# Kernel tuning notes

Hardware: AMD Instinct MI355X
Metric: run time of the kernel (lower is better)

The kernel has to match this reference:

```python
import jax, jax.numpy as jnp
import numpy as np

B, C, H, W = 4, 512, 64, 64
CI = C // 2  # inter_channel


def setup_inputs() -> dict:
    key = jax.random.key(0)
    ks = jax.random.split(key, 5)
    x = jax.random.normal(ks[0], (B, C, H, W), dtype=jnp.float32)
    # 1x1 convs with bias=False == channel-mixing matrices (out_ch, in_ch)
    w_phi = jax.random.normal(ks[1], (CI, C), dtype=jnp.float32) * 0.02
    w_theta = jax.random.normal(ks[2], (CI, C), dtype=jnp.float32) * 0.02
    w_g = jax.random.normal(ks[3], (CI, C), dtype=jnp.float32) * 0.02
    w_mask = jax.random.normal(ks[4], (C, CI), dtype=jnp.float32) * 0.02
    return {"x": x, "w_phi": w_phi, "w_theta": w_theta, "w_g": w_g, "w_mask": w_mask}


def reference(x, w_phi, w_theta, w_g, w_mask):
    b, c, h, w = x.shape
    n = h * w
    ci = w_phi.shape[0]
    xf = x.reshape(b, c, n)  # (b, c, N)
    # 1x1 convs as channel matmuls -> (b, ci, N)
    phi = jnp.einsum('oc,bcn->bon', w_phi, xf)
    theta = jnp.einsum('oc,bcn->bon', w_theta, xf)
    g = jnp.einsum('oc,bcn->bon', w_g, xf)
    # f = theta^T @ phi : (b, N, N), unscaled scores
    f = jnp.einsum('bcn,bcm->bnm', theta, phi)
    a = jax.nn.softmax(f, axis=-1)
    # y = a @ g^T, produced directly in (b, ci, N) layout (fuses the permute)
    y = jnp.einsum('bnm,bcm->bcn', a, g)
    # conv_mask: 1x1 conv back to C channels
    out = jnp.einsum('oc,bcn->bon', w_mask, y)
    return out.reshape(b, c, h, w)
```

## Files before the change

kernel.cpp:

```cpp
#include <hip/hip_runtime.h>


#define BB 4
#define CC 512
#define NN_SP 4096
#define CI 256

typedef _Float16 f16x8 __attribute__((ext_vector_type(8)));
typedef float f32x4 __attribute__((ext_vector_type(4)));

__device__ __forceinline__ void async16(const void* gsrc, void* ldst) {
  __builtin_amdgcn_global_load_lds(
      (const __attribute__((address_space(1))) unsigned int*)gsrc,
      (__attribute__((address_space(3))) unsigned int*)ldst, 16, 0, 0);
}

__global__ __launch_bounds__(256) void convert_w(
    const float* __restrict__ wphi, const float* __restrict__ wtheta,
    const float* __restrict__ wg, const float* __restrict__ wmask,
    _Float16* __restrict__ wpt, _Float16* __restrict__ wgh, _Float16* __restrict__ wmh) {
  int i = blockIdx.x * 256 + threadIdx.x;
  if (i < 512 * 512) {
    int row = i >> 9, k = i & 511;
    float v = (row < 256) ? wphi[row * 512 + k] : wtheta[(row - 256) * 512 + k];
    wpt[i] = (_Float16)v;
  } else if (i < 512 * 512 + 256 * 512) {
    int j = i - 512 * 512;
    wgh[j] = (_Float16)wg[j];
  } else {
    int j = i - 512 * 512 - 256 * 512;
    wmh[j] = (_Float16)wmask[j];
  }
}

__global__ __launch_bounds__(256) void transpose_x(const float* __restrict__ x,
                                                   _Float16* __restrict__ xT) {
  __shared__ float tile[64][65];
  const int n0 = blockIdx.x * 64, c0 = blockIdx.y * 64, b = blockIdx.z;
  const int tx = threadIdx.x & 63, ty = threadIdx.x >> 6;
  const float* xb = x + (long long)b * CC * NN_SP;
#pragma unroll
  for (int i = 0; i < 16; ++i) {
    int row = i * 4 + ty;
    tile[row][tx] = xb[(long long)(c0 + row) * NN_SP + n0 + tx];
  }
  __syncthreads();
  const int cx = threadIdx.x & 31;
  const int ny = threadIdx.x >> 5;
  _Float16* xTb = xT + (long long)b * NN_SP * CC;
#pragma unroll
  for (int i = 0; i < 8; ++i) {
    int n = i * 8 + ny;
    union { _Float16 h[2]; unsigned int u; } pk;
    pk.h[0] = (_Float16)tile[cx * 2][n];
    pk.h[1] = (_Float16)tile[cx * 2 + 1][n];
    *(unsigned int*)(xTb + (long long)(n0 + n) * CC + c0 + cx * 2) = pk.u;
  }
}

template <int M, int NT, int K, bool F16OUT>
__global__ __launch_bounds__(256, 2) void gemm_bt(
    const _Float16* __restrict__ Ab, const _Float16* __restrict__ Btb,
    void* __restrict__ Cb, long long sA, long long sB, long long sC) {
  __shared__ _Float16 As[128 * 64];
  __shared__ _Float16 Bs[128 * 64];
  const int tid = threadIdx.x, lane = tid & 63, w = tid >> 6;
  const int wm = w >> 1, wn = w & 1;
  const int l15 = lane & 15, lq = lane >> 4;
  const int b = blockIdx.z;
  const _Float16* A = Ab + (long long)b * sA;
  const _Float16* Bt = Btb + (long long)b * sB;
  const int m0 = blockIdx.y * 128, n0 = blockIdx.x * 128;

  f32x4 acc[4][4];
#pragma unroll
  for (int i = 0; i < 4; ++i)
#pragma unroll
    for (int j = 0; j < 4; ++j) acc[i][j] = (f32x4){0.f, 0.f, 0.f, 0.f};

  for (int k0 = 0; k0 < K; k0 += 64) {
    __syncthreads();
#pragma unroll
    for (int j = 0; j < 4; ++j) {
      int chw = j * 256 + w * 64;
      int ch = chw + lane;
      int us = ch ^ ((ch >> 3) & 7);
      int row = us >> 3, kc = us & 7;
      async16(A + (long long)(m0 + row) * K + k0 + kc * 8, (void*)(As + chw * 8));
      async16(Bt + (long long)(n0 + row) * K + k0 + kc * 8, (void*)(Bs + chw * 8));
    }
    __syncthreads();
#pragma unroll
    for (int kh = 0; kh < 2; ++kh) {
      f16x8 af[4], bf[4];
#pragma unroll
      for (int mt = 0; mt < 4; ++mt) {
        int c = (wm * 64 + mt * 16 + l15) * 8 + kh * 4 + lq;
        af[mt] = *(const f16x8*)(As + (c ^ ((c >> 3) & 7)) * 8);
      }
#pragma unroll
      for (int nt = 0; nt < 4; ++nt) {
        int c = (wn * 64 + nt * 16 + l15) * 8 + kh * 4 + lq;
        bf[nt] = *(const f16x8*)(Bs + (c ^ ((c >> 3) & 7)) * 8);
      }
#pragma unroll
      for (int mt = 0; mt < 4; ++mt)
#pragma unroll
        for (int nt = 0; nt < 4; ++nt)
          acc[mt][nt] = __builtin_amdgcn_mfma_f32_16x16x32_f16(af[mt], bf[nt], acc[mt][nt], 0, 0, 0);
    }
  }

#pragma unroll
  for (int mt = 0; mt < 4; ++mt)
#pragma unroll
    for (int nt = 0; nt < 4; ++nt)
#pragma unroll
      for (int r = 0; r < 4; ++r) {
        int row = m0 + wm * 64 + mt * 16 + lq * 4 + r;
        int col = n0 + wn * 64 + nt * 16 + l15;
        if (F16OUT)
          ((_Float16*)Cb + (long long)b * sC)[(long long)row * NT + col] = (_Float16)acc[mt][nt][r];
        else
          ((float*)Cb + (long long)b * sC)[(long long)row * NT + col] = acc[mt][nt][r];
      }
}

__global__ __launch_bounds__(512, 2) void flash_attn3(
    const _Float16* __restrict__ pt, const _Float16* __restrict__ g,
    _Float16* __restrict__ yT) {
  __shared__ _Float16 Stg[2][2][16384];
  __shared__ _Float16 Ps[8][2048];
  const int tid = threadIdx.x, lane = tid & 63, w = tid >> 6;
  const int hw = w >> 2, wp = w & 3;
  const int l15 = lane & 15, lq = lane >> 4;

  const int idx = blockIdx.x;
  const int b = (idx >> 1) & 3;
  const int q0 = (((idx >> 3) << 1) | (idx & 1)) * 64;
  const int kvbase = hw * 2048;
  const _Float16* __restrict__ ptb = pt + (long long)b * NN_SP * 512;
  const _Float16* __restrict__ gb = g + (long long)b * CI * NN_SP;

  int offPhi[4], offG[4], chw_[4];
#pragma unroll
  for (int j = 0; j < 4; ++j) {
    int u = wp * 256 + j * 64 + lane;
    chw_[j] = wp * 256 + j * 64;
    int us = u ^ ((u >> 3) & 7);
    int k2 = us >> 9, nv8 = (us >> 6) & 7, r15 = (us >> 2) & 15, rq = us & 3;
    offPhi[j] = (nv8 * 16 + r15) * 512 + k2 * 32 + rq * 8;
    int kq = us >> 8, ct4 = (us >> 6) & 3;
    offG[j] = (ct4 * 16 + r15) * 4096 + kq * 32 + rq * 8;
  }
  const int rswz = (l15 * 4 + lq) ^ ((l15 >> 1) & 7);

  f16x8 qreg[8];
#pragma unroll
  for (int kk = 0; kk < 8; ++kk)
    qreg[kk] = *(const f16x8*)(
        ptb + (long long)(q0 + wp * 16 + l15) * 512 + 256 + kk * 32 + lq * 8);

  f16x8 onesf;
#pragma unroll
  for (int j = 0; j < 8; ++j) onesf[j] = (_Float16)1.f;

  f32x4 yacc[16];
#pragma unroll
  for (int nt = 0; nt < 16; ++nt) yacc[nt] = (f32x4){0.f, 0.f, 0.f, 0.f};
  f32x4 lacc = (f32x4){0.f, 0.f, 0.f, 0.f};
  float mrow[4] = {-3e38f, -3e38f, -3e38f, -3e38f};

  auto issue = [&](int mq, int bi) {
    if (mq >= 64) return;
    int t = mq >> 2, mp = mq & 3, kv0 = kvbase + t * 128;
#pragma unroll
    for (int hh = 0; hh < 2; ++hh) {
      int sub = mp * 2 + hh;
      _Float16* buf = Stg[hw][bi] + hh * 8192;
      if (sub < 4) {
        const _Float16* basep = ptb + (long long)kv0 * 512 + sub * 64;
#pragma unroll
        for (int j = 0; j < 4; ++j)
          async16(basep + offPhi[j], (void*)(buf + chw_[j] * 8));
      } else {
        const _Float16* baseg = gb + (long long)(sub - 4) * 64 * 4096 + kv0;
#pragma unroll
        for (int j = 0; j < 4; ++j)
          async16(baseg + offG[j], (void*)(buf + chw_[j] * 8));
      }
    }
  };

  int p = 0;
  issue(0, 0);

  for (int t = 0; t < 16; ++t) {
    f32x4 S[8];
#pragma unroll
    for (int i = 0; i < 8; ++i) S[i] = (f32x4){0.f, 0.f, 0.f, 0.f};

#pragma unroll
    for (int mp = 0; mp < 2; ++mp) {
      asm volatile("s_waitcnt vmcnt(0)" ::: "memory");
      asm volatile("s_barrier" ::: "memory");
      issue(p + 1, (p + 1) & 1);
      const _Float16* bufb = Stg[hw][p & 1];
      __builtin_amdgcn_s_setprio(1);
#pragma unroll
      for (int hh = 0; hh < 2; ++hh) {
        int c = mp * 2 + hh;
        const _Float16* buf = bufb + hh * 8192;
#pragma unroll
        for (int k2 = 0; k2 < 2; ++k2)
#pragma unroll
          for (int nv = 0; nv < 8; ++nv) {
            f16x8 bf = *(const f16x8*)(buf + (k2 * 512 + nv * 64 + rswz) * 8);
            S[nv] = __builtin_amdgcn_mfma_f32_16x16x32_f16(qreg[c * 2 + k2], bf, S[nv], 0, 0, 0);
          }
      }
      __builtin_amdgcn_s_setprio(0);
      ++p;
    }

    float nm[4];
    int grew = 0;
#pragma unroll
    for (int r = 0; r < 4; ++r) {
      float mx = fmaxf(fmaxf(S[0][r], S[1][r]), fmaxf(S[2][r], S[3][r]));
      mx = fmaxf(mx, fmaxf(fmaxf(S[4][r], S[5][r]), fmaxf(S[6][r], S[7][r])));
#pragma unroll
      for (int d = 1; d < 16; d <<= 1) mx = fmaxf(mx, __shfl_xor(mx, d, 64));
      nm[r] = fmaxf(mrow[r], mx);
      grew |= (mx > mrow[r]);
    }
    if (__ballot(grew)) {
      f32x4 al;
#pragma unroll
      for (int r = 0; r < 4; ++r) {
        al[r] = __expf(mrow[r] - nm[r]);
        mrow[r] = nm[r];
      }
#pragma unroll
      for (int nt = 0; nt < 16; ++nt) yacc[nt] *= al;
      lacc *= al;
    }
#pragma unroll
    for (int r = 0; r < 4; ++r)
#pragma unroll
      for (int nv = 0; nv < 8; ++nv) S[nv][r] = __expf(S[nv][r] - mrow[r]);

#pragma unroll
    for (int nv = 0; nv < 8; ++nv) {
      int kq = nv >> 1;
      int lqr = (nv & 1) * 2 + (l15 >> 3);
      int e = l15 & 7;
#pragma unroll
      for (int r = 0; r < 4; ++r) {
        int u = kq * 64 + lqr * 16 + lq * 4 + r;
        int us = u ^ ((u >> 3) & 7);
        Ps[w][us * 8 + e] = (_Float16)S[nv][r];
      }
    }
    f16x8 aP[4];
#pragma unroll
    for (int kq = 0; kq < 4; ++kq) {
      int ur = kq * 64 + lane;
      int urs = ur ^ ((ur >> 3) & 7);
      aP[kq] = *(const f16x8*)(&Ps[w][urs * 8]);
    }

#pragma unroll
    for (int kq = 0; kq < 4; ++kq)
      lacc = __builtin_amdgcn_mfma_f32_16x16x32_f16(aP[kq], onesf, lacc, 0, 0, 0);

#pragma unroll
    for (int mp = 0; mp < 2; ++mp) {
      asm volatile("s_waitcnt vmcnt(0)" ::: "memory");
      asm volatile("s_barrier" ::: "memory");
      issue(p + 1, (p + 1) & 1);
      const _Float16* bufb = Stg[hw][p & 1];
      __builtin_amdgcn_s_setprio(1);
#pragma unroll
      for (int hh = 0; hh < 2; ++hh) {
        int cg = mp * 2 + hh;
        const _Float16* buf = bufb + hh * 8192;
#pragma unroll
        for (int kq = 0; kq < 4; ++kq)
#pragma unroll
          for (int ct = 0; ct < 4; ++ct) {
            f16x8 bf = *(const f16x8*)(buf + (kq * 256 + ct * 64 + rswz) * 8);
            yacc[cg * 4 + ct] =
                __builtin_amdgcn_mfma_f32_16x16x32_f16(aP[kq], bf, yacc[cg * 4 + ct], 0, 0, 0);
          }
      }
      __builtin_amdgcn_s_setprio(0);
      ++p;
    }
  }

  __syncthreads();
  float* mbuf = (float*)Stg;
  float* sbuf = (float*)((char*)Stg + 81920);
  if (hw == 1) {
#pragma unroll
    for (int r = 0; r < 4; ++r) {
      int rr = wp * 16 + lq * 4 + r;
#pragma unroll
      for (int nt = 0; nt < 16; ++nt)
        mbuf[rr * 257 + nt * 16 + l15] = yacc[nt][r];
      if (l15 == 0) {
        sbuf[rr * 2 + 0] = mrow[r];
        sbuf[rr * 2 + 1] = lacc[r];
      }
    }
  }
  __syncthreads();
  if (hw == 0) {
    _Float16* yTb = yT + (long long)b * NN_SP * CI;
#pragma unroll
    for (int r = 0; r < 4; ++r) {
      int rr = wp * 16 + lq * 4 + r;
      float m2 = sbuf[rr * 2 + 0], l2 = sbuf[rr * 2 + 1];
      float m = fmaxf(mrow[r], m2);
      float w1 = __expf(mrow[r] - m), w2 = __expf(m2 - m);
      float inv = 1.f / (w1 * lacc[r] + w2 * l2);
      int row = q0 + rr;
#pragma unroll
      for (int nt = 0; nt < 16; ++nt) {
        float v2 = mbuf[rr * 257 + nt * 16 + l15];
        yTb[(long long)row * CI + nt * 16 + l15] =
            (_Float16)((w1 * yacc[nt][r] + w2 * v2) * inv);
      }
    }
  }
}

extern "C" void kernel_launch(void* const* d_in, const int* in_sizes, int n_in,
                              void* d_out, int out_size, void* d_ws, size_t ws_size,
                              hipStream_t stream) {
  const float* x = (const float*)d_in[0];
  const float* w_phi = (const float*)d_in[1];
  const float* w_theta = (const float*)d_in[2];
  const float* w_g = (const float*)d_in[3];
  const float* w_mask = (const float*)d_in[4];
  float* out = (float*)d_out;
  char* ws = (char*)d_ws;

  _Float16* xT = (_Float16*)(ws);
  _Float16* pt = (_Float16*)(ws + 16777216);
  _Float16* gB = (_Float16*)(ws + 33554432);
  _Float16* yT = (_Float16*)(ws + 41943040);
  _Float16* wpt = (_Float16*)(ws + 50331648);
  _Float16* wg = (_Float16*)(ws + 50855936);
  _Float16* wm = (_Float16*)(ws + 51118080);

  convert_w<<<2048, 256, 0, stream>>>(w_phi, w_theta, w_g, w_mask, wpt, wg, wm);
  transpose_x<<<dim3(64, 8, 4), 256, 0, stream>>>(x, xT);
  gemm_bt<4096, 512, 512, true><<<dim3(4, 32, 4), 256, 0, stream>>>(
      xT, wpt, pt, 4096LL * 512, 0, 4096LL * 512);
  gemm_bt<256, 4096, 512, true><<<dim3(32, 2, 4), 256, 0, stream>>>(
      wg, xT, gB, 0, 4096LL * 512, 256LL * 4096);
  flash_attn3<<<dim3(256), 512, 0, stream>>>(pt, gB, yT);
  gemm_bt<512, 4096, 256, false><<<dim3(32, 4, 4), 256, 0, stream>>>(
      wm, yT, out, 0, 4096LL * 256, 512LL * 4096);
}
```

Measured before the change: 240.7 us.

## Stagger flash-attention phases between wave halves to overlap softmax with MFMA

Flattens the per-tile loop into a single 66-step loop in which the second half of the waves (hw=1) runs two sub-steps behind the first. One half's softmax (max, exp, P store) then coincides with the other half's MFMA work, spreading VALU and matrix pressure across the block. Buffer selection moves to the step parity, and S/aP become loop-carried state. The cost is two extra barrier steps and more branching inside the loop, which may hurt code scheduling or raise register pressure.

```diff
diff --git a/kernel.cpp b/kernel.cpp
--- a/kernel.cpp
+++ b/kernel.cpp
@@ -170,14 +170,20 @@
   for (int nt = 0; nt < 16; ++nt) yacc[nt] = (f32x4){0.f, 0.f, 0.f, 0.f};
   f32x4 lacc = (f32x4){0.f, 0.f, 0.f, 0.f};
   float mrow[4] = {-3e38f, -3e38f, -3e38f, -3e38f};
-
-  auto issue = [&](int mq, int bi) {
-    if (mq >= 64) return;
+  f32x4 S[8];
+#pragma unroll
+  for (int i = 0; i < 8; ++i) S[i] = (f32x4){0.f, 0.f, 0.f, 0.f};
+  f16x8 aP[4];
+#pragma unroll
+  for (int kq = 0; kq < 4; ++kq) aP[kq] = onesf;
+
+  auto issue = [&](int mq) {
+    if (mq < 0 || mq >= 64) return;
     int t = mq >> 2, mp = mq & 3, kv0 = kvbase + t * 128;
 #pragma unroll
     for (int hh = 0; hh < 2; ++hh) {
       int sub = mp * 2 + hh;
-      _Float16* buf = Stg[hw][bi] + hh * 8192;
+      _Float16* buf = Stg[hw][mq & 1] + hh * 8192;
       if (sub < 4) {
         const _Float16* basep = ptb + (long long)kv0 * 512 + sub * 64;
 #pragma unroll
@@ -192,110 +198,102 @@
     }
   };
 
-  int p = 0;
-  issue(0, 0);
-
-  for (int t = 0; t < 16; ++t) {
-    f32x4 S[8];
-#pragma unroll
-    for (int i = 0; i < 8; ++i) S[i] = (f32x4){0.f, 0.f, 0.f, 0.f};
-
-#pragma unroll
-    for (int mp = 0; mp < 2; ++mp) {
-      asm volatile("s_waitcnt vmcnt(0)" ::: "memory");
-      asm volatile("s_barrier" ::: "memory");
-      issue(p + 1, (p + 1) & 1);
-      const _Float16* bufb = Stg[hw][p & 1];
-      __builtin_amdgcn_s_setprio(1);
-#pragma unroll
-      for (int hh = 0; hh < 2; ++hh) {
-        int c = mp * 2 + hh;
-        const _Float16* buf = bufb + hh * 8192;
-#pragma unroll
-        for (int k2 = 0; k2 < 2; ++k2)
+  issue(hw == 0 ? 0 : -1);
+
+  for (int iv = 0; iv < 66; ++iv) {
+    const int lp = iv - 2 * hw;
+    asm volatile("s_waitcnt vmcnt(0)" ::: "memory");
+    asm volatile("s_barrier" ::: "memory");
+    issue(lp + 1);
+    if (lp >= 0 && lp < 64) {
+      const _Float16* bufb = Stg[hw][lp & 1];
+      const int ph = lp & 3;
+      if (ph < 2) {
+        if (ph == 0) {
+#pragma unroll
+          for (int i = 0; i < 8; ++i) S[i] = (f32x4){0.f, 0.f, 0.f, 0.f};
+        }
+        __builtin_amdgcn_s_setprio(1);
+#pragma unroll
+        for (int hh = 0; hh < 2; ++hh) {
+          int c = ph * 2 + hh;
+          const _Float16* buf = bufb + hh * 8192;
+#pragma unroll
+          for (int k2 = 0; k2 < 2; ++k2)
+#pragma unroll
+            for (int nv = 0; nv < 8; ++nv) {
+              f16x8 bf = *(const f16x8*)(buf + (k2 * 512 + nv * 64 + rswz) * 8);
+              S[nv] = __builtin_amdgcn_mfma_f32_16x16x32_f16(qreg[c * 2 + k2], bf, S[nv], 0, 0, 0);
+            }
+        }
+        __builtin_amdgcn_s_setprio(0);
+        if (ph == 1) {
+          float nm[4];
+          int grew = 0;
+#pragma unroll
+          for (int r = 0; r < 4; ++r) {
+            float mx = fmaxf(fmaxf(S[0][r], S[1][r]), fmaxf(S[2][r], S[3][r]));
+            mx = fmaxf(mx, fmaxf(fmaxf(S[4][r], S[5][r]), fmaxf(S[6][r], S[7][r])));
+#pragma unroll
+            for (int d = 1; d < 16; d <<= 1) mx = fmaxf(mx, __shfl_xor(mx, d, 64));
+            nm[r] = fmaxf(mrow[r], mx);
+            grew |= (mx > mrow[r]);
+          }
+          if (__ballot(grew)) {
+            f32x4 al;
+#pragma unroll
+            for (int r = 0; r < 4; ++r) {
+              al[r] = __expf(mrow[r] - nm[r]);
+              mrow[r] = nm[r];
+            }
+#pragma unroll
+            for (int nt = 0; nt < 16; ++nt) yacc[nt] *= al;
+            lacc *= al;
+          }
+#pragma unroll
+          for (int r = 0; r < 4; ++r)
+#pragma unroll
+            for (int nv = 0; nv < 8; ++nv) S[nv][r] = __expf(S[nv][r] - mrow[r]);
+
 #pragma unroll
           for (int nv = 0; nv < 8; ++nv) {
-            f16x8 bf = *(const f16x8*)(buf + (k2 * 512 + nv * 64 + rswz) * 8);
-            S[nv] = __builtin_amdgcn_mfma_f32_16x16x32_f16(qreg[c * 2 + k2], bf, S[nv], 0, 0, 0);
+            int kq = nv >> 1;
+            int lqr = (nv & 1) * 2 + (l15 >> 3);
+            int e = l15 & 7;
+#pragma unroll
+            for (int r = 0; r < 4; ++r) {
+              int u = kq * 64 + lqr * 16 + lq * 4 + r;
+              int us = u ^ ((u >> 3) & 7);
+              Ps[w][us * 8 + e] = (_Float16)S[nv][r];
+            }
           }
-      }
-      __builtin_amdgcn_s_setprio(0);
-      ++p;
-    }
-
-    float nm[4];
-    int grew = 0;
-#pragma unroll
-    for (int r = 0; r < 4; ++r) {
-      float mx = fmaxf(fmaxf(S[0][r], S[1][r]), fmaxf(S[2][r], S[3][r]));
-      mx = fmaxf(mx, fmaxf(fmaxf(S[4][r], S[5][r]), fmaxf(S[6][r], S[7][r])));
-#pragma unroll
-      for (int d = 1; d < 16; d <<= 1) mx = fmaxf(mx, __shfl_xor(mx, d, 64));
-      nm[r] = fmaxf(mrow[r], mx);
-      grew |= (mx > mrow[r]);
-    }
-    if (__ballot(grew)) {
-      f32x4 al;
-#pragma unroll
-      for (int r = 0; r < 4; ++r) {
-        al[r] = __expf(mrow[r] - nm[r]);
-        mrow[r] = nm[r];
-      }
-#pragma unroll
-      for (int nt = 0; nt < 16; ++nt) yacc[nt] *= al;
-      lacc *= al;
-    }
-#pragma unroll
-    for (int r = 0; r < 4; ++r)
-#pragma unroll
-      for (int nv = 0; nv < 8; ++nv) S[nv][r] = __expf(S[nv][r] - mrow[r]);
-
-#pragma unroll
-    for (int nv = 0; nv < 8; ++nv) {
-      int kq = nv >> 1;
-      int lqr = (nv & 1) * 2 + (l15 >> 3);
-      int e = l15 & 7;
-#pragma unroll
-      for (int r = 0; r < 4; ++r) {
-        int u = kq * 64 + lqr * 16 + lq * 4 + r;
-        int us = u ^ ((u >> 3) & 7);
-        Ps[w][us * 8 + e] = (_Float16)S[nv][r];
-      }
-    }
-    f16x8 aP[4];
-#pragma unroll
-    for (int kq = 0; kq < 4; ++kq) {
-      int ur = kq * 64 + lane;
-      int urs = ur ^ ((ur >> 3) & 7);
-      aP[kq] = *(const f16x8*)(&Ps[w][urs * 8]);
-    }
-
-#pragma unroll
-    for (int kq = 0; kq < 4; ++kq)
-      lacc = __builtin_amdgcn_mfma_f32_16x16x32_f16(aP[kq], onesf, lacc, 0, 0, 0);
-
-#pragma unroll
-    for (int mp = 0; mp < 2; ++mp) {
-      asm volatile("s_waitcnt vmcnt(0)" ::: "memory");
-      asm volatile("s_barrier" ::: "memory");
-      issue(p + 1, (p + 1) & 1);
-      const _Float16* bufb = Stg[hw][p & 1];
-      __builtin_amdgcn_s_setprio(1);
-#pragma unroll
-      for (int hh = 0; hh < 2; ++hh) {
-        int cg = mp * 2 + hh;
-        const _Float16* buf = bufb + hh * 8192;
-#pragma unroll
-        for (int kq = 0; kq < 4; ++kq)
-#pragma unroll
-          for (int ct = 0; ct < 4; ++ct) {
-            f16x8 bf = *(const f16x8*)(buf + (kq * 256 + ct * 64 + rswz) * 8);
-            yacc[cg * 4 + ct] =
-                __builtin_amdgcn_mfma_f32_16x16x32_f16(aP[kq], bf, yacc[cg * 4 + ct], 0, 0, 0);
+#pragma unroll
+          for (int kq = 0; kq < 4; ++kq) {
+            int ur = kq * 64 + lane;
+            int urs = ur ^ ((ur >> 3) & 7);
+            aP[kq] = *(const f16x8*)(&Ps[w][urs * 8]);
           }
-      }
-      __builtin_amdgcn_s_setprio(0);
-      ++p;
+#pragma unroll
+          for (int kq = 0; kq < 4; ++kq)
+            lacc = __builtin_amdgcn_mfma_f32_16x16x32_f16(aP[kq], onesf, lacc, 0, 0, 0);
+        }
+      } else {
+        __builtin_amdgcn_s_setprio(1);
+#pragma unroll
+        for (int hh = 0; hh < 2; ++hh) {
+          int cg = (ph - 2) * 2 + hh;
+          const _Float16* buf = bufb + hh * 8192;
+#pragma unroll
+          for (int kq = 0; kq < 4; ++kq)
+#pragma unroll
+            for (int ct = 0; ct < 4; ++ct) {
+              f16x8 bf = *(const f16x8*)(buf + (kq * 256 + ct * 64 + rswz) * 8);
+              yacc[cg * 4 + ct] =
+                  __builtin_amdgcn_mfma_f32_16x16x32_f16(aP[kq], bf, yacc[cg * 4 + ct], 0, 0, 0);
+            }
+        }
+        __builtin_amdgcn_s_setprio(0);
+      }
     }
   }
 
```

Measured after the change: 490.8 us. 2.04x slower.

## Double-buffer GEMM K loads and triple-buffer flash attention KV stages

Applied to the files above, without the earlier changes.

The projection GEMM now double-buffers its A/B shared-memory tiles, prefetching the next K chunk while it computes on the current one and dropping one of two barriers per iteration. The attention kernel switches from two 32KB stages to three 16KB stages at finer granularity, issuing loads two stages ahead and waiting only for older loads with vmcnt(4). This is meant to hide global-to-LDS latency behind MFMA work. GEMM shared memory doubles to 64KB, which may limit occupancy at 2 blocks per CU.

```diff
diff --git a/kernel.cpp b/kernel.cpp
--- a/kernel.cpp
+++ b/kernel.cpp
@@ -62,8 +62,8 @@
 __global__ __launch_bounds__(256, 2) void gemm_bt(
     const _Float16* __restrict__ Ab, const _Float16* __restrict__ Btb,
     void* __restrict__ Cb, long long sA, long long sB, long long sC) {
-  __shared__ _Float16 As[128 * 64];
-  __shared__ _Float16 Bs[128 * 64];
+  __shared__ _Float16 As[2][128 * 64];
+  __shared__ _Float16 Bs[2][128 * 64];
   const int tid = threadIdx.x, lane = tid & 63, w = tid >> 6;
   const int wm = w >> 1, wn = w & 1;
   const int l15 = lane & 15, lq = lane >> 4;
@@ -78,30 +78,36 @@
 #pragma unroll
     for (int j = 0; j < 4; ++j) acc[i][j] = (f32x4){0.f, 0.f, 0.f, 0.f};
 
-  for (int k0 = 0; k0 < K; k0 += 64) {
-    __syncthreads();
+  auto stage = [&](int k0, int bi) {
 #pragma unroll
     for (int j = 0; j < 4; ++j) {
       int chw = j * 256 + w * 64;
       int ch = chw + lane;
       int us = ch ^ ((ch >> 3) & 7);
       int row = us >> 3, kc = us & 7;
-      async16(A + (long long)(m0 + row) * K + k0 + kc * 8, (void*)(As + chw * 8));
-      async16(Bt + (long long)(n0 + row) * K + k0 + kc * 8, (void*)(Bs + chw * 8));
-    }
-    __syncthreads();
+      async16(A + (long long)(m0 + row) * K + k0 + kc * 8, (void*)(As[bi] + chw * 8));
+      async16(Bt + (long long)(n0 + row) * K + k0 + kc * 8, (void*)(Bs[bi] + chw * 8));
+    }
+  };
+
+  stage(0, 0);
+  for (int it = 0; it < K / 64; ++it) {
+    const int cur = it & 1;
+    asm volatile("s_waitcnt vmcnt(0)" ::: "memory");
+    asm volatile("s_barrier" ::: "memory");
+    if (it + 1 < K / 64) stage((it + 1) * 64, cur ^ 1);
 #pragma unroll
     for (int kh = 0; kh < 2; ++kh) {
       f16x8 af[4], bf[4];
 #pragma unroll
       for (int mt = 0; mt < 4; ++mt) {
         int c = (wm * 64 + mt * 16 + l15) * 8 + kh * 4 + lq;
-        af[mt] = *(const f16x8*)(As + (c ^ ((c >> 3) & 7)) * 8);
+        af[mt] = *(const f16x8*)(As[cur] + (c ^ ((c >> 3) & 7)) * 8);
       }
 #pragma unroll
       for (int nt = 0; nt < 4; ++nt) {
         int c = (wn * 64 + nt * 16 + l15) * 8 + kh * 4 + lq;
-        bf[nt] = *(const f16x8*)(Bs + (c ^ ((c >> 3) & 7)) * 8);
+        bf[nt] = *(const f16x8*)(Bs[cur] + (c ^ ((c >> 3) & 7)) * 8);
       }
 #pragma unroll
       for (int mt = 0; mt < 4; ++mt)
@@ -129,7 +135,7 @@
 __global__ __launch_bounds__(512, 2) void flash_attn3(
     const _Float16* __restrict__ pt, const _Float16* __restrict__ g,
     _Float16* __restrict__ yT) {
-  __shared__ _Float16 Stg[2][2][16384];
+  __shared__ _Float16 Stg[2][3][8192];
   __shared__ _Float16 Ps[8][2048];
   const int tid = threadIdx.x, lane = tid & 63, w = tid >> 6;
   const int hw = w >> 2, wp = w & 3;
@@ -171,29 +177,26 @@
   f32x4 lacc = (f32x4){0.f, 0.f, 0.f, 0.f};
   float mrow[4] = {-3e38f, -3e38f, -3e38f, -3e38f};
 
-  auto issue = [&](int mq, int bi) {
-    if (mq >= 64) return;
-    int t = mq >> 2, mp = mq & 3, kv0 = kvbase + t * 128;
-#pragma unroll
-    for (int hh = 0; hh < 2; ++hh) {
-      int sub = mp * 2 + hh;
-      _Float16* buf = Stg[hw][bi] + hh * 8192;
-      if (sub < 4) {
-        const _Float16* basep = ptb + (long long)kv0 * 512 + sub * 64;
-#pragma unroll
-        for (int j = 0; j < 4; ++j)
-          async16(basep + offPhi[j], (void*)(buf + chw_[j] * 8));
-      } else {
-        const _Float16* baseg = gb + (long long)(sub - 4) * 64 * 4096 + kv0;
-#pragma unroll
-        for (int j = 0; j < 4; ++j)
-          async16(baseg + offG[j], (void*)(buf + chw_[j] * 8));
-      }
+  auto issue = [&](int q, int bi) {
+    if (q >= 128) return;
+    _Float16* buf = Stg[hw][bi];
+    int tq = q >> 3, sub = q & 7, kv0 = kvbase + tq * 128;
+    if (sub < 4) {
+      const _Float16* basep = ptb + (long long)kv0 * 512 + sub * 64;
+#pragma unroll
+      for (int j = 0; j < 4; ++j)
+        async16(basep + offPhi[j], (void*)(buf + chw_[j] * 8));
+    } else {
+      const _Float16* baseg = gb + (long long)(sub - 4) * 64 * 4096 + kv0;
+#pragma unroll
+      for (int j = 0; j < 4; ++j)
+        async16(baseg + offG[j], (void*)(buf + chw_[j] * 8));
     }
   };
 
-  int p = 0;
+  int p = 0, bcur = 0;
   issue(0, 0);
+  issue(1, 1);
 
   for (int t = 0; t < 16; ++t) {
     f32x4 S[8];
@@ -201,26 +204,22 @@
     for (int i = 0; i < 8; ++i) S[i] = (f32x4){0.f, 0.f, 0.f, 0.f};
 
 #pragma unroll
-    for (int mp = 0; mp < 2; ++mp) {
-      asm volatile("s_waitcnt vmcnt(0)" ::: "memory");
+    for (int c = 0; c < 4; ++c) {
+      asm volatile("s_waitcnt vmcnt(4)" ::: "memory");
       asm volatile("s_barrier" ::: "memory");
-      issue(p + 1, (p + 1) & 1);
-      const _Float16* bufb = Stg[hw][p & 1];
+      int bn = bcur + 2; if (bn >= 3) bn -= 3;
+      issue(p + 2, bn);
+      const _Float16* buf = Stg[hw][bcur];
       __builtin_amdgcn_s_setprio(1);
 #pragma unroll
-      for (int hh = 0; hh < 2; ++hh) {
-        int c = mp * 2 + hh;
-        const _Float16* buf = bufb + hh * 8192;
-#pragma unroll
-        for (int k2 = 0; k2 < 2; ++k2)
-#pragma unroll
-          for (int nv = 0; nv < 8; ++nv) {
-            f16x8 bf = *(const f16x8*)(buf + (k2 * 512 + nv * 64 + rswz) * 8);
-            S[nv] = __builtin_amdgcn_mfma_f32_16x16x32_f16(qreg[c * 2 + k2], bf, S[nv], 0, 0, 0);
-          }
-      }
+      for (int k2 = 0; k2 < 2; ++k2)
+#pragma unroll
+        for (int nv = 0; nv < 8; ++nv) {
+          f16x8 bf = *(const f16x8*)(buf + (k2 * 512 + nv * 64 + rswz) * 8);
+          S[nv] = __builtin_amdgcn_mfma_f32_16x16x32_f16(qreg[c * 2 + k2], bf, S[nv], 0, 0, 0);
+        }
       __builtin_amdgcn_s_setprio(0);
-      ++p;
+      ++p; ++bcur; if (bcur == 3) bcur = 0;
     }
 
     float nm[4];
@@ -275,27 +274,27 @@
       lacc = __builtin_amdgcn_mfma_f32_16x16x32_f16(aP[kq], onesf, lacc, 0, 0, 0);
 
 #pragma unroll
-    for (int mp = 0; mp < 2; ++mp) {
-      asm volatile("s_waitcnt vmcnt(0)" ::: "memory");
+    for (int cg = 0; cg < 4; ++cg) {
+      if (t == 15 && cg == 3) {
+        asm volatile("s_waitcnt vmcnt(0)" ::: "memory");
+      } else {
+        asm volatile("s_waitcnt vmcnt(4)" ::: "memory");
+      }
       asm volatile("s_barrier" ::: "memory");
-      issue(p + 1, (p + 1) & 1);
-      const _Float16* bufb = Stg[hw][p & 1];
+      int bn = bcur + 2; if (bn >= 3) bn -= 3;
+      issue(p + 2, bn);
+      const _Float16* buf = Stg[hw][bcur];
       __builtin_amdgcn_s_setprio(1);
 #pragma unroll
-      for (int hh = 0; hh < 2; ++hh) {
-        int cg = mp * 2 + hh;
-        const _Float16* buf = bufb + hh * 8192;
-#pragma unroll
-        for (int kq = 0; kq < 4; ++kq)
-#pragma unroll
-          for (int ct = 0; ct < 4; ++ct) {
-            f16x8 bf = *(const f16x8*)(buf + (kq * 256 + ct * 64 + rswz) * 8);
-            yacc[cg * 4 + ct] =
-                __builtin_amdgcn_mfma_f32_16x16x32_f16(aP[kq], bf, yacc[cg * 4 + ct], 0, 0, 0);
-          }
-      }
+      for (int kq = 0; kq < 4; ++kq)
+#pragma unroll
+        for (int ct = 0; ct < 4; ++ct) {
+          f16x8 bf = *(const f16x8*)(buf + (kq * 256 + ct * 64 + rswz) * 8);
+          yacc[cg * 4 + ct] =
+              __builtin_amdgcn_mfma_f32_16x16x32_f16(aP[kq], bf, yacc[cg * 4 + ct], 0, 0, 0);
+        }
       __builtin_amdgcn_s_setprio(0);
-      ++p;
+      ++p; ++bcur; if (bcur == 3) bcur = 0;
     }
   }
 
```

After: 274.5 us. 14.1% more time.
